# Performance work log

Measured on AMD Instinct MI355X. Metric: run time of the kernel, lower is better.

## Reference

```python
import jax, jax.numpy as jnp
from jax import lax
import numpy as np

PROPRIO = 48
NPTS = 1024
NP_PROX = 512
NP_DIST = 512
HP = 187  # proximal_feature_dim
HD = 64   # distal_feature_dim
B = 2048
NA = 12
ACTOR_DIMS = [PROPRIO + HP + HD, 1024, 512, 256, 128, NA]


def gru_last(x, wih, whh, bih, bhh):
    """torch-style GRU (gate order r,z,n), returns last hidden. x: [B,T,in]."""
    Bx, T, _ = x.shape
    H = whh.shape[1]
    gx = x @ wih.T + bih  # [B,T,3H], input projections precomputed
    def step(h, gxt):
        gh = h @ whh.T + bhh
        r = jax.nn.sigmoid(gxt[:, :H] + gh[:, :H])
        z = jax.nn.sigmoid(gxt[:, H:2 * H] + gh[:, H:2 * H])
        n = jnp.tanh(gxt[:, 2 * H:] + r * gh[:, 2 * H:])
        return (1.0 - z) * n + z * h, None
    h0 = jnp.zeros((Bx, H), x.dtype)
    hT, _ = lax.scan(step, h0, jnp.swapaxes(gx, 0, 1))
    return hT


def _encode(pts, w1, b1, w2, b2):
    h = jax.nn.elu(pts @ w1.T + b1)
    return jax.nn.elu(h @ w2.T + b2)


def _forward(obs, pe_prox_w1, pe_prox_b1, pe_prox_w2, pe_prox_b2,
             pe_dist_w1, pe_dist_b1, pe_dist_w2, pe_dist_b2,
             gru_prox_wih, gru_prox_whh, gru_prox_bih, gru_prox_bhh,
             gru_dist_wih, gru_dist_whh, gru_dist_bih, gru_dist_bhh,
             mem_prox_wih, mem_prox_whh, mem_prox_bih, mem_prox_bhh,
             mem_dist_wih, mem_dist_whh, mem_dist_bih, mem_dist_bhh,
             actor_w0, actor_b0, actor_w1, actor_b1, actor_w2, actor_b2,
             actor_w3, actor_b3, actor_w4, actor_b4,
             prox_idx, dist_idx):
    proprio = obs[:, :PROPRIO]
    lidar = obs[:, PROPRIO:].reshape(obs.shape[0], NPTS, 3)  # history_length=1
    # irregular gather of proximal/distal point subsets (sampling plan buffers)
    prox_enc = _encode(lidar[:, prox_idx], pe_prox_w1, pe_prox_b1, pe_prox_w2, pe_prox_b2)  # [B,512,64]
    dist_enc = _encode(lidar[:, dist_idx], pe_dist_w1, pe_dist_b1, pe_dist_w2, pe_dist_b2)  # [B,512,64]
    # spatial GRUs over the point sequence
    hp = gru_last(prox_enc, gru_prox_wih, gru_prox_whh, gru_prox_bih, gru_prox_bhh)  # [B,187]
    hd = gru_last(dist_enc, gru_dist_wih, gru_dist_whh, gru_dist_bih, gru_dist_bhh)  # [B,64]
    # temporal memory GRUs (single step, zero initial hidden)
    fp = gru_last(hp[:, None, :], mem_prox_wih, mem_prox_whh, mem_prox_bih, mem_prox_bhh)
    fd = gru_last(hd[:, None, :], mem_dist_wih, mem_dist_whh, mem_dist_bih, mem_dist_bhh)
    x = jnp.concatenate([proprio, fp, fd], axis=-1)  # [B,299]
    for w, b in ((actor_w0, actor_b0), (actor_w1, actor_b1), (actor_w2, actor_b2), (actor_w3, actor_b3)):
        x = jax.nn.elu(x @ w.T + b)
    return x @ actor_w4.T + actor_b4  # action mean [B,12]


def setup_inputs() -> dict:
    key = jax.random.key(0)
    ks = iter(jax.random.split(key, 64))
    def n(shape, scale=0.05):
        return (jax.random.normal(next(ks), shape, jnp.float32) * scale)
    inp = {}
    inp["obs"] = jax.random.normal(next(ks), (B, PROPRIO + NPTS * 3), jnp.float32)
    inp["prox_idx"] = jax.random.randint(next(ks), (NP_PROX,), 0, NPTS)
    inp["dist_idx"] = jax.random.randint(next(ks), (NP_DIST,), 0, NPTS)
    for pfx in ("pe_prox", "pe_dist"):
        inp[pfx + "_w1"] = n((64, 3)); inp[pfx + "_b1"] = jnp.zeros((64,), jnp.float32)
        inp[pfx + "_w2"] = n((64, 64)); inp[pfx + "_b2"] = jnp.zeros((64,), jnp.float32)
    for pfx, H, din in (("gru_prox", HP, 64), ("gru_dist", HD, 64), ("mem_prox", HP, HP), ("mem_dist", HD, HD)):
        inp[pfx + "_wih"] = n((3 * H, din)); inp[pfx + "_whh"] = n((3 * H, H))
        inp[pfx + "_bih"] = jnp.zeros((3 * H,), jnp.float32); inp[pfx + "_bhh"] = jnp.zeros((3 * H,), jnp.float32)
    for i, (di, do) in enumerate(zip(ACTOR_DIMS[:-1], ACTOR_DIMS[1:])):
        inp[f"actor_w{i}"] = n((do, di)); inp[f"actor_b{i}"] = jnp.zeros((do,), jnp.float32)
    return inp


def reference(obs, prox_idx, dist_idx,
              pe_prox_w1, pe_prox_b1, pe_prox_w2, pe_prox_b2,
              pe_dist_w1, pe_dist_b1, pe_dist_w2, pe_dist_b2,
              gru_prox_wih, gru_prox_whh, gru_prox_bih, gru_prox_bhh,
              gru_dist_wih, gru_dist_whh, gru_dist_bih, gru_dist_bhh,
              mem_prox_wih, mem_prox_whh, mem_prox_bih, mem_prox_bhh,
              mem_dist_wih, mem_dist_whh, mem_dist_bih, mem_dist_bhh,
              actor_w0, actor_b0, actor_w1, actor_b1, actor_w2, actor_b2,
              actor_w3, actor_b3, actor_w4, actor_b4):
    return _forward(obs, pe_prox_w1, pe_prox_b1, pe_prox_w2, pe_prox_b2,
                    pe_dist_w1, pe_dist_b1, pe_dist_w2, pe_dist_b2,
                    gru_prox_wih, gru_prox_whh, gru_prox_bih, gru_prox_bhh,
                    gru_dist_wih, gru_dist_whh, gru_dist_bih, gru_dist_bhh,
                    mem_prox_wih, mem_prox_whh, mem_prox_bih, mem_prox_bhh,
                    mem_dist_wih, mem_dist_whh, mem_dist_bih, mem_dist_bhh,
                    actor_w0, actor_b0, actor_w1, actor_b1, actor_w2, actor_b2,
                    actor_w3, actor_b3, actor_w4, actor_b4,
                    prox_idx, dist_idx)
```

## Files before the change

kernel.cpp:

```cpp
#include <hip/hip_runtime.h>
#include <stdint.h>

typedef __attribute__((ext_vector_type(8))) short short8;
typedef __attribute__((ext_vector_type(4))) float f32x4;
typedef __attribute__((ext_vector_type(4))) unsigned int u32x4;

#define DEV __device__ __forceinline__

#define L2E 1.4426950408889634f

DEV unsigned short f2bf(float f) {
    union { float f; uint32_t u; } v; v.f = f;
    return (unsigned short)((v.u + 0x7FFFu + ((v.u >> 16) & 1u)) >> 16);
}
DEV uint8_t f2fp8(float f) {
    union { float f; uint32_t u; } v; v.f = f;
    uint32_t s = (v.u >> 24) & 0x80u;
    uint32_t absu = v.u & 0x7FFFFFFFu;
    int E = (int)(absu >> 23);
    if (E >= 135 + 1) return (uint8_t)(s | 0x7E);
    if (E >= 121) {
        uint32_t m = absu & 0x7FFFFFu;
        uint32_t keep = m >> 20;
        uint32_t rest = m & 0xFFFFFu;
        uint32_t rnd = (rest > 0x80000u || (rest == 0x80000u && (keep & 1u))) ? 1u : 0u;
        uint32_t mag = (((uint32_t)(E - 120) << 3) | keep) + rnd;
        if (mag > 0x7Eu) mag = 0x7Eu;
        return (uint8_t)(s | mag);
    }
    float sc = __builtin_fabsf(f) * 512.f;
    uint32_t m8 = (uint32_t)(sc + 0.5f);
    if (m8 > 7u) return (uint8_t)(s | 0x08);
    return (uint8_t)(s | m8);
}
DEV float sig_(float x) {
    return __builtin_amdgcn_rcpf(1.f + __builtin_amdgcn_exp2f(-L2E * x));
}
DEV float tanh_(float x) {
    return 1.f - 2.f * __builtin_amdgcn_rcpf(1.f + __builtin_amdgcn_exp2f(2.f * L2E * x));
}
DEV float elu_(float x) {
    return x > 0.f ? x : __builtin_amdgcn_exp2f(L2E * x) - 1.f;
}
DEV f32x4 splat4(float v) { f32x4 r; r[0]=v; r[1]=v; r[2]=v; r[3]=v; return r; }
DEV void pin(short8& v) { asm volatile("" : "+v"(v)); }
DEV void pinl(long& v)  { asm volatile("" : "+v"(v)); }

struct PJob { const float* s; unsigned short* d; int Hs, NG, Ks, Kd, total; };
struct PJobs { PJob j[12]; };

__global__ __launch_bounds__(256) void pack_all(PJobs P)
{
    PJob jb = P.j[blockIdx.y];
    int e = blockIdx.x * 256 + threadIdx.x;
    if (e >= jb.total) return;
    int n = e / jb.Kd, k = e - n * jb.Kd;
    int g = n / jb.NG, jj = n - g * jb.NG;
    float v = (jj < jb.Hs && k < jb.Ks) ? jb.s[(size_t)(g * jb.Hs + jj) * jb.Ks + k] : 0.f;
    jb.d[e] = f2bf(v);
}

__global__ __launch_bounds__(256) void pack_fp8(const float* __restrict__ src,
                                                uint8_t* __restrict__ dst)
{
    int e = blockIdx.x * 256 + threadIdx.x;
    if (e >= 576 * 64) return;
    int n = e >> 6, k = e & 63;
    int g = n / 192, jj = n - g * 192;
    float v = (jj < 187) ? src[(size_t)(g * 187 + jj) * 64 + k] : 0.f;
    dst[e] = f2fp8(v);
}

__global__ __launch_bounds__(256) void enc_kernel(
    const float* __restrict__ obs, const int* __restrict__ idx,
    const float* __restrict__ w1, const float* __restrict__ b1,
    const unsigned short* __restrict__ w2p, const float* __restrict__ b2,
    uint8_t* __restrict__ enc8)
{
    const int b = blockIdx.x, t0 = blockIdx.y * 64;
    const int tid = threadIdx.x;
    __shared__ __align__(16) float pts[64][4];
    __shared__ float w1s[256];
    __shared__ float b1s[64], b2s[64];
    __shared__ __align__(16) unsigned short h1s[64][72];

    if (tid < 192) w1s[(tid/3)*4 + (tid - (tid/3)*3)] = w1[tid];
    if (tid < 64) { b1s[tid] = b1[tid]; b2s[tid] = b2[tid]; }
    for (int e = tid; e < 192; e += 256) {
        int p = e / 3, c2 = e - p * 3;
        int pi = idx[t0 + p];
        pts[p][c2] = obs[(size_t)b * 3120 + 48 + (size_t)pi * 3 + c2];
    }
    __syncthreads();
#pragma unroll
    for (int r = 0; r < 16; ++r) {
        int e = tid + r * 256;
        int p = e >> 6, ch = e & 63;
        float v = w1s[ch*4]*pts[p][0] + w1s[ch*4+1]*pts[p][1]
                + w1s[ch*4+2]*pts[p][2] + b1s[ch];
        h1s[p][ch] = f2bf(elu_(v));
    }
    __syncthreads();
    const int wave = tid >> 6, lane = tid & 63, quad = lane >> 4, l16 = lane & 15;
#pragma unroll
    for (int ct = 0; ct < 4; ++ct) {
        f32x4 a2 = splat4(0.f);
#pragma unroll
        for (int ks = 0; ks < 2; ++ks) {
            short8 af = *(const short8*)(&h1s[wave*16 + l16][ks*32 + quad*8]);
            short8 bf = *(const short8*)(w2p + (ct*16 + l16)*64 + ks*32 + quad*8);
            a2 = __builtin_amdgcn_mfma_f32_16x16x32_bf16(af, bf, a2, 0, 0, 0);
        }
        int c = ct*16 + l16;
        float b2v = b2s[c];
#pragma unroll
        for (int j = 0; j < 4; ++j) {
            int m = wave*16 + quad*4 + j;
            enc8[((size_t)b*512 + t0 + m)*64 + c] = f2fp8(elu_(a2[j] + b2v));
        }
    }
}

DEV void gru_body_pre(int blk, const uint8_t* __restrict__ enc8,
                      const uint8_t* __restrict__ wih8,
                      const unsigned short* __restrict__ whh,
                      const float* __restrict__ bih, const float* __restrict__ bhh,
                      unsigned short* __restrict__ houtb, char* smem)
{
    constexpr int H = 187, KP = 192, KS = 6, HP8 = 200;
    unsigned short* hlds = (unsigned short*)smem;
    uint8_t* xs = (uint8_t*)(smem + 12800);

    const int tid  = threadIdx.x;
    const int wave = tid >> 6, lane = tid & 63, quad = lane >> 4, l16 = lane & 15;
    const int b0   = blk * 16;
    const int c    = wave * 16 + l16;

    for (int e = tid; e < 2*16*HP8; e += 768) hlds[e] = 0;

    short8 whr[3][KS];
    long   wx8[3][2];
#pragma unroll
    for (int g = 0; g < 3; ++g) {
#pragma unroll
        for (int ks = 0; ks < KS; ++ks)
            whr[g][ks] = *(const short8*)(whh + ((size_t)(g*KP + c))*KP + ks*32 + quad*8);
#pragma unroll
        for (int ks = 0; ks < 2; ++ks)
            wx8[g][ks] = *(const long*)(wih8 + ((size_t)(g*KP + c))*64 + ks*32 + quad*8);
    }
#pragma unroll
    for (int g = 0; g < 3; ++g) {
#pragma unroll
        for (int ks = 0; ks < KS; ++ks) pin(whr[g][ks]);
#pragma unroll
        for (int ks = 0; ks < 2; ++ks)  pinl(wx8[g][ks]);
    }
    float bsr = 0.f, bsz = 0.f, binx = 0.f, bhnn = 0.f;
    if (c < H) {
        bsr  = bih[c]       + bhh[c];
        bsz  = bih[H + c]   + bhh[H + c];
        binx = bih[2*H + c];
        bhnn = bhh[2*H + c];
    }
    float hreg[4] = {0.f, 0.f, 0.f, 0.f};

    u32x4 xq;
    const int xrow = lane >> 2, xseg = lane & 3;
    if (wave == 0) {
        xq = *(const u32x4*)(enc8 + ((size_t)(b0 + xrow)*512 + 0)*64 + xseg*16);
        *(u32x4*)(xs + 0*1280 + xrow*80 + xseg*16) = xq;
        xq = *(const u32x4*)(enc8 + ((size_t)(b0 + xrow)*512 + 1)*64 + xseg*16);
    }
    __syncthreads();

    int cur = 0;
    for (int t = 0; t < 512; ++t) {
        if (wave == 0) {
            *(u32x4*)(xs + ((t+1)&1)*1280 + xrow*80 + xseg*16) = xq;
            int tn = (t + 2 < 512) ? t + 2 : 511;
            xq = *(const u32x4*)(enc8 + ((size_t)(b0 + xrow)*512 + tn)*64 + xseg*16);
        }
        const uint8_t* xsr = xs + (t&1)*1280;
        const unsigned short* hc = hlds + cur * (16*HP8);
        unsigned short*       hn = hlds + (cur ^ 1) * (16*HP8);

        f32x4 acc[4];
        acc[0] = splat4(bsr);
        acc[1] = splat4(bsz);
        acc[2] = splat4(binx);
        acc[3] = splat4(bhnn);
#pragma unroll
        for (int ks = 0; ks < 2; ++ks) {
            long a8 = *(const long*)(xsr + l16*80 + ks*32 + quad*8);
            acc[0] = __builtin_amdgcn_mfma_f32_16x16x32_fp8_fp8(a8, wx8[0][ks], acc[0], 0, 0, 0);
            acc[1] = __builtin_amdgcn_mfma_f32_16x16x32_fp8_fp8(a8, wx8[1][ks], acc[1], 0, 0, 0);
            acc[2] = __builtin_amdgcn_mfma_f32_16x16x32_fp8_fp8(a8, wx8[2][ks], acc[2], 0, 0, 0);
        }
#pragma unroll
        for (int ks = 0; ks < KS; ++ks) {
            short8 ah = *(const short8*)(hc + l16*HP8 + ks*32 + quad*8);
            acc[0] = __builtin_amdgcn_mfma_f32_16x16x32_bf16(ah, whr[0][ks], acc[0], 0, 0, 0);
            acc[1] = __builtin_amdgcn_mfma_f32_16x16x32_bf16(ah, whr[1][ks], acc[1], 0, 0, 0);
            acc[3] = __builtin_amdgcn_mfma_f32_16x16x32_bf16(ah, whr[2][ks], acc[3], 0, 0, 0);
        }
#pragma unroll
        for (int j = 0; j < 4; ++j) {
            int m = quad*4 + j;
            float r  = sig_(acc[0][j]);
            float zg = sig_(acc[1][j]);
            float nn = tanh_(acc[2][j] + r * acc[3][j]);
            float hv = nn + zg * (hreg[j] - nn);
            hreg[j] = hv;
            hn[m*HP8 + c] = f2bf(hv);
        }
        cur ^= 1;
        __syncthreads();
    }
#pragma unroll
    for (int j = 0; j < 4; ++j) {
        int m = quad*4 + j;
        houtb[(size_t)(b0 + m)*KP + c] = (c < H) ? f2bf(hreg[j]) : 0;
    }
}

template<int H, int KP>
DEV void gru_body_fused(int blk,
                  const float* __restrict__ obs, const int* __restrict__ idx,
                  const float* __restrict__ w1, const float* __restrict__ b1,
                  const float* __restrict__ w2, const float* __restrict__ b2,
                  const unsigned short* __restrict__ wih, const unsigned short* __restrict__ whh,
                  const float* __restrict__ bih, const float* __restrict__ bhh,
                  unsigned short* __restrict__ houtb, char* smem)
{
    constexpr int NCT = KP / 16;
    constexpr int KS  = KP / 32;
    constexpr int HP8 = KP + 8;

    unsigned short* hlds = (unsigned short*)(smem);
    unsigned short* xs   = (unsigned short*)(smem + 12800);
    unsigned short* h1s  = (unsigned short*)(smem + 17408);
    unsigned short* w2s  = (unsigned short*)(smem + 22016);
    float* ptsb          = (float*)(smem + 31232);
    float* w1s           = (float*)(smem + 31744);
    float* b1s           = (float*)(smem + 32768);
    float* b2s           = (float*)(smem + 33024);

    const int tid  = threadIdx.x;
    const int wave = tid >> 6, lane = tid & 63, quad = lane >> 4, l16 = lane & 15;
    const int b0   = blk * 16;
    const int ct   = wave;
    const bool act = (ct < NCT);
    const int c    = ct * 16 + l16;

    for (int e = tid; e < 2*16*HP8; e += 768) hlds[e] = 0;
    for (int e = tid; e < 4096; e += 768) { int n = e >> 6, k = e & 63; w2s[n*72 + k] = f2bf(w2[e]); }
    if (tid < 192) w1s[(tid/3)*4 + (tid - (tid/3)*3)] = w1[tid];
    if (tid < 64) { b1s[tid] = b1[tid]; b2s[tid] = b2[tid]; }

    const float* myrow = obs + (size_t)(b0 + (tid & 15)) * 3120 + 48;
    float px = 0.f, py = 0.f, pz = 0.f;
    if (tid < 16) {
        int p0 = idx[0];
        ptsb[tid*4 + 0] = myrow[3*p0 + 0];
        ptsb[tid*4 + 1] = myrow[3*p0 + 1];
        ptsb[tid*4 + 2] = myrow[3*p0 + 2];
        int p1 = idx[1];
        px = myrow[3*p1 + 0]; py = myrow[3*p1 + 1]; pz = myrow[3*p1 + 2];
    }

    short8 whr[3][KS];
    short8 wxr[3][2];
    float bsr = 0.f, bsz = 0.f, binx = 0.f, bhnn = 0.f;
    {
        const int cl = act ? c : l16;
#pragma unroll
        for (int g = 0; g < 3; ++g) {
#pragma unroll
            for (int ks = 0; ks < KS; ++ks)
                whr[g][ks] = *(const short8*)(whh + ((size_t)(g*KP + cl))*KP + ks*32 + quad*8);
#pragma unroll
            for (int ks = 0; ks < 2; ++ks)
                wxr[g][ks] = *(const short8*)(wih + ((size_t)(g*KP + cl))*64 + ks*32 + quad*8);
        }
    }
#pragma unroll
    for (int g = 0; g < 3; ++g) {
#pragma unroll
        for (int ks = 0; ks < KS; ++ks) pin(whr[g][ks]);
#pragma unroll
        for (int ks = 0; ks < 2; ++ks)  pin(wxr[g][ks]);
    }
    if (act && c < H) {
        bsr  = bih[c]       + bhh[c];
        bsz  = bih[H + c]   + bhh[H + c];
        binx = bih[2*H + c];
        bhnn = bhh[2*H + c];
    }
    float hreg[4] = {0.f, 0.f, 0.f, 0.f};

    __syncthreads();

    int cur = 0;
    for (int i = 0; i < 514; ++i) {
        if (i < 512) {
            const float* pt = ptsb + (i & 1) * 64;
            unsigned short* h1w = h1s + (i & 1) * (16*72);
#pragma unroll
            for (int e = tid; e < 1024; e += 768) {
                int p = e >> 6, ch = e & 63;
                float v = w1s[ch*4+0]*pt[p*4+0] + w1s[ch*4+1]*pt[p*4+1]
                        + w1s[ch*4+2]*pt[p*4+2] + b1s[ch];
                h1w[p*72 + ch] = f2bf(elu_(v));
            }
            if (tid < 16) {
                float* dst = ptsb + ((i+1) & 1) * 64 + tid*4;
                dst[0] = px; dst[1] = py; dst[2] = pz;
                int tn = (i + 2 < 512) ? i + 2 : 511;
                int pn = idx[tn];
                px = myrow[3*pn + 0]; py = myrow[3*pn + 1]; pz = myrow[3*pn + 2];
            }
        }
        if (i >= 1 && i < 513 && wave < 4) {
            const unsigned short* h1r = h1s + ((i-1) & 1) * (16*72);
            unsigned short*       xw  = xs  + ((i-1) & 1) * (16*72);
            f32x4 a2 = splat4(0.f);
#pragma unroll
            for (int ks = 0; ks < 2; ++ks) {
                short8 af = *(const short8*)(h1r + l16*72 + ks*32 + quad*8);
                short8 bf = *(const short8*)(w2s + (wave*16 + l16)*72 + ks*32 + quad*8);
                a2 = __builtin_amdgcn_mfma_f32_16x16x32_bf16(af, bf, a2, 0, 0, 0);
            }
            int c2 = wave*16 + l16;
            float b2v = b2s[c2];
#pragma unroll
            for (int j = 0; j < 4; ++j)
                xw[(quad*4 + j)*72 + c2] = f2bf(elu_(a2[j] + b2v));
        }
        if (i >= 2) {
            int t = i - 2;
            const unsigned short* xsr = xs + (t & 1) * (16*72);
            const unsigned short* hc  = hlds + cur * (16*HP8);
            unsigned short*       hn  = hlds + (cur ^ 1) * (16*HP8);
            if (act) {
                f32x4 acc[4];
                acc[0] = splat4(bsr);
                acc[1] = splat4(bsz);
                acc[2] = splat4(binx);
                acc[3] = splat4(bhnn);
#pragma unroll
                for (int ks = 0; ks < 2; ++ks) {
                    short8 xf = *(const short8*)(xsr + l16*72 + ks*32 + quad*8);
                    acc[0] = __builtin_amdgcn_mfma_f32_16x16x32_bf16(xf, wxr[0][ks], acc[0], 0, 0, 0);
                    acc[1] = __builtin_amdgcn_mfma_f32_16x16x32_bf16(xf, wxr[1][ks], acc[1], 0, 0, 0);
                    acc[2] = __builtin_amdgcn_mfma_f32_16x16x32_bf16(xf, wxr[2][ks], acc[2], 0, 0, 0);
                }
#pragma unroll
                for (int ks = 0; ks < KS; ++ks) {
                    short8 ah = *(const short8*)(hc + l16*HP8 + ks*32 + quad*8);
                    acc[0] = __builtin_amdgcn_mfma_f32_16x16x32_bf16(ah, whr[0][ks], acc[0], 0, 0, 0);
                    acc[1] = __builtin_amdgcn_mfma_f32_16x16x32_bf16(ah, whr[1][ks], acc[1], 0, 0, 0);
                    acc[3] = __builtin_amdgcn_mfma_f32_16x16x32_bf16(ah, whr[2][ks], acc[3], 0, 0, 0);
                }
#pragma unroll
                for (int j = 0; j < 4; ++j) {
                    int m = quad*4 + j;
                    float r  = sig_(acc[0][j]);
                    float zg = sig_(acc[1][j]);
                    float nn = tanh_(acc[2][j] + r * acc[3][j]);
                    float hv = nn + zg * (hreg[j] - nn);
                    hreg[j] = hv;
                    hn[m*HP8 + c] = f2bf(hv);
                }
            }
            cur ^= 1;
        }
        __syncthreads();
    }

    if (act)
#pragma unroll
        for (int j = 0; j < 4; ++j) {
            int m = quad*4 + j;
            houtb[(size_t)(b0 + m)*KP + c] = (c < H) ? f2bf(hreg[j]) : 0;
        }
}

__global__ __launch_bounds__(768) void gru_kernel(
    int mode,
    const float* __restrict__ obs,
    const int* __restrict__ prox_idx, const int* __restrict__ dist_idx,
    const uint8_t* __restrict__ encp8, const uint8_t* __restrict__ wihp8,
    const float* __restrict__ w1p, const float* __restrict__ b1p,
    const float* __restrict__ w2p, const float* __restrict__ b2p,
    const float* __restrict__ w1d, const float* __restrict__ b1d,
    const float* __restrict__ w2d, const float* __restrict__ b2d,
    const unsigned short* __restrict__ wihp, const unsigned short* __restrict__ whhp,
    const unsigned short* __restrict__ wihd, const unsigned short* __restrict__ whhd,
    const float* __restrict__ bihp, const float* __restrict__ bhhp,
    const float* __restrict__ bihd, const float* __restrict__ bhhd,
    unsigned short* __restrict__ hpb, unsigned short* __restrict__ hdb)
{
    __shared__ __align__(16) char smem[33280];
    if (blockIdx.x < 128) {
        if (mode == 0)
            gru_body_pre(blockIdx.x, encp8, wihp8, whhp, bihp, bhhp, hpb, smem);
        else
            gru_body_fused<187, 192>(blockIdx.x, obs, prox_idx, w1p, b1p, w2p, b2p,
                                     wihp, whhp, bihp, bhhp, hpb, smem);
    } else {
        gru_body_fused<64, 64>(blockIdx.x - 128, obs, dist_idx, w1d, b1d, w2d, b2d,
                               wihd, whhd, bihd, bhhd, hdb, smem);
    }
}

__global__ __launch_bounds__(256) void bgemm_kernel(
    const unsigned short* __restrict__ A, const unsigned short* __restrict__ B,
    const float* __restrict__ bias, void* __restrict__ C,
    int Kp, int Np, int Nstore, int mode)
{
    __shared__ __align__(16) unsigned short Asl[64*40];
    __shared__ __align__(16) unsigned short Bsl[64*40];
    const int tid = threadIdx.x;
    const int wave = tid >> 6, lane = tid & 63, quad = lane >> 4, l16 = lane & 15;
    const int n0 = blockIdx.x * 64, m0 = blockIdx.y * 64;
    const int r = tid >> 2, sg = (tid & 3) * 8;

    f32x4 acc[4];
#pragma unroll
    for (int nt = 0; nt < 4; ++nt) acc[nt] = splat4(0.f);

    for (int k0 = 0; k0 < Kp; k0 += 32) {
        short8 av = *(const short8*)(A + (size_t)(m0 + r)*Kp + k0 + sg);
        short8 bv;
        if (n0 + r < Np) bv = *(const short8*)(B + (size_t)(n0 + r)*Kp + k0 + sg);
        else { short8 z; for (int q = 0; q < 8; ++q) z[q] = 0; bv = z; }
        *(short8*)(Asl + r*40 + sg) = av;
        *(short8*)(Bsl + r*40 + sg) = bv;
        __syncthreads();
        short8 af = *(const short8*)(Asl + (wave*16 + l16)*40 + quad*8);
#pragma unroll
        for (int nt = 0; nt < 4; ++nt) {
            short8 bf = *(const short8*)(Bsl + (nt*16 + l16)*40 + quad*8);
            acc[nt] = __builtin_amdgcn_mfma_f32_16x16x32_bf16(af, bf, acc[nt], 0, 0, 0);
        }
        __syncthreads();
    }
#pragma unroll
    for (int nt = 0; nt < 4; ++nt) {
        int n = n0 + nt*16 + l16;
        float bv = (bias && n < Np) ? bias[n] : 0.f;
#pragma unroll
        for (int j = 0; j < 4; ++j) {
            int m = m0 + wave*16 + quad*4 + j;
            float v = acc[nt][j] + bv;
            if (mode == 1) {
                ((unsigned short*)C)[(size_t)m*Np + n] = f2bf(elu_(v));
            } else {
                if (n < Nstore) ((float*)C)[(size_t)m*Nstore + n] = v;
            }
        }
    }
}

__global__ __launch_bounds__(256) void memcat_kernel(
    const float* __restrict__ obs, const float* __restrict__ Gp, const float* __restrict__ Gd,
    const float* __restrict__ mbip, const float* __restrict__ mbhp,
    const float* __restrict__ mbid, const float* __restrict__ mbhd,
    unsigned short* __restrict__ x0b)
{
    int i = blockIdx.x * 256 + threadIdx.x;
    if (i >= 2048 * 320) return;
    int b = i / 320, cc = i - b * 320;
    float v;
    if (cc < 48) {
        v = obs[(size_t)b*3120 + cc];
    } else if (cc < 235) {
        int j = cc - 48;
        float dr = Gp[(size_t)b*576 + j];
        float dz = Gp[(size_t)b*576 + 192 + j];
        float dn = Gp[(size_t)b*576 + 384 + j];
        float r  = sig_(dr + mbip[j] + mbhp[j]);
        float zg = sig_(dz + mbip[187+j] + mbhp[187+j]);
        float nn = tanh_(dn + mbip[374+j] + r * mbhp[374+j]);
        v = (1.f - zg) * nn;
    } else if (cc < 299) {
        int j = cc - 235;
        float dr = Gd[(size_t)b*192 + j];
        float dz = Gd[(size_t)b*192 + 64 + j];
        float dn = Gd[(size_t)b*192 + 128 + j];
        float r  = sig_(dr + mbid[j] + mbhd[j]);
        float zg = sig_(dz + mbid[64+j] + mbhd[64+j]);
        float nn = tanh_(dn + mbid[128+j] + r * mbhd[128+j]);
        v = (1.f - zg) * nn;
    } else {
        v = 0.f;
    }
    x0b[i] = f2bf(v);
}

extern "C" void kernel_launch(void* const* d_in, const int* in_sizes, int n_in,
                              void* d_out, int out_size, void* d_ws, size_t ws_size,
                              hipStream_t stream)
{
    (void)in_sizes; (void)n_in; (void)out_size;
    const float* obs        = (const float*)d_in[0];
    const int*   prox_idx   = (const int*)d_in[1];
    const int*   dist_idx   = (const int*)d_in[2];
    const float* pe_prox_w1 = (const float*)d_in[3];
    const float* pe_prox_b1 = (const float*)d_in[4];
    const float* pe_prox_w2 = (const float*)d_in[5];
    const float* pe_prox_b2 = (const float*)d_in[6];
    const float* pe_dist_w1 = (const float*)d_in[7];
    const float* pe_dist_b1 = (const float*)d_in[8];
    const float* pe_dist_w2 = (const float*)d_in[9];
    const float* pe_dist_b2 = (const float*)d_in[10];
    const float* gp_wih = (const float*)d_in[11];
    const float* gp_whh = (const float*)d_in[12];
    const float* gp_bih = (const float*)d_in[13];
    const float* gp_bhh = (const float*)d_in[14];
    const float* gd_wih = (const float*)d_in[15];
    const float* gd_whh = (const float*)d_in[16];
    const float* gd_bih = (const float*)d_in[17];
    const float* gd_bhh = (const float*)d_in[18];
    const float* mp_wih = (const float*)d_in[19];
    const float* mp_bih = (const float*)d_in[21];
    const float* mp_bhh = (const float*)d_in[22];
    const float* md_wih = (const float*)d_in[23];
    const float* md_bih = (const float*)d_in[25];
    const float* md_bhh = (const float*)d_in[26];
    const float* aw0 = (const float*)d_in[27]; const float* ab0 = (const float*)d_in[28];
    const float* aw1 = (const float*)d_in[29]; const float* ab1 = (const float*)d_in[30];
    const float* aw2 = (const float*)d_in[31]; const float* ab2 = (const float*)d_in[32];
    const float* aw3 = (const float*)d_in[33]; const float* ab3 = (const float*)d_in[34];
    const float* aw4 = (const float*)d_in[35]; const float* ab4 = (const float*)d_in[36];
    float* out = (float*)d_out;

    char* ws = (char*)d_ws;
    size_t off = 0;
    auto alloc = [&](size_t bytes) -> char* {
        char* p = ws + off;
        off = (off + bytes + 255) & ~(size_t)255;
        return p;
    };
    unsigned short* wih_p = (unsigned short*)alloc(36864*2);
    unsigned short* whh_p = (unsigned short*)alloc(110592*2);
    unsigned short* wih_d = (unsigned short*)alloc(12288*2);
    unsigned short* whh_d = (unsigned short*)alloc(12288*2);
    unsigned short* mw_p  = (unsigned short*)alloc(110592*2);
    unsigned short* mw_d  = (unsigned short*)alloc(12288*2);
    unsigned short* w0p   = (unsigned short*)alloc((size_t)1024*320*2);
    unsigned short* w1p   = (unsigned short*)alloc((size_t)512*1024*2);
    unsigned short* w2p   = (unsigned short*)alloc((size_t)256*512*2);
    unsigned short* w3p   = (unsigned short*)alloc((size_t)128*256*2);
    unsigned short* w4p   = (unsigned short*)alloc((size_t)16*128*2);
    unsigned short* w2e   = (unsigned short*)alloc(4096*2);
    uint8_t* wih8         = (uint8_t*)alloc(576*64);
    unsigned short* hpb   = (unsigned short*)alloc((size_t)2048*192*2);
    unsigned short* hdb   = (unsigned short*)alloc((size_t)2048*64*2);
    float* Gp             = (float*)alloc((size_t)2048*576*4);
    float* Gd             = (float*)alloc((size_t)2048*192*4);
    unsigned short* x0b   = (unsigned short*)alloc((size_t)2048*320*2);
    unsigned short* a1b   = (unsigned short*)alloc((size_t)2048*1024*2);
    unsigned short* a2b   = (unsigned short*)alloc((size_t)2048*512*2);
    unsigned short* a3b   = (unsigned short*)alloc((size_t)2048*256*2);
    unsigned short* a4b   = (unsigned short*)alloc((size_t)2048*128*2);
    uint8_t* enc8         = (uint8_t*)alloc((size_t)2048*512*64);
    const int mode = (off <= ws_size) ? 0 : 1;

    PJobs P;
    P.j[0]  = { gp_wih, wih_p, 187, 192, 64, 64, 36864 };
    P.j[1]  = { gp_whh, whh_p, 187, 192, 187, 192, 110592 };
    P.j[2]  = { gd_wih, wih_d, 64, 64, 64, 64, 12288 };
    P.j[3]  = { gd_whh, whh_d, 64, 64, 64, 64, 12288 };
    P.j[4]  = { mp_wih, mw_p, 187, 192, 187, 192, 110592 };
    P.j[5]  = { md_wih, mw_d, 64, 64, 64, 64, 12288 };
    P.j[6]  = { aw0, w0p, 1024, 1024, 299, 320, 327680 };
    P.j[7]  = { aw1, w1p, 512, 512, 1024, 1024, 524288 };
    P.j[8]  = { aw2, w2p, 256, 256, 512, 512, 131072 };
    P.j[9]  = { aw3, w3p, 128, 128, 256, 256, 32768 };
    P.j[10] = { aw4, w4p, 12, 16, 128, 128, 2048 };
    P.j[11] = { pe_prox_w2, w2e, 64, 64, 64, 64, 4096 };
    pack_all<<<dim3(2048, 12), 256, 0, stream>>>(P);

    if (mode == 0) {
        pack_fp8<<<144, 256, 0, stream>>>(gp_wih, wih8);
        enc_kernel<<<dim3(2048, 8), 256, 0, stream>>>(
            obs, prox_idx, pe_prox_w1, pe_prox_b1, w2e, pe_prox_b2, enc8);
    }

    gru_kernel<<<256, 768, 0, stream>>>(
        mode, obs, prox_idx, dist_idx, enc8, wih8,
        pe_prox_w1, pe_prox_b1, pe_prox_w2, pe_prox_b2,
        pe_dist_w1, pe_dist_b1, pe_dist_w2, pe_dist_b2,
        wih_p, whh_p, wih_d, whh_d,
        gp_bih, gp_bhh, gd_bih, gd_bhh, hpb, hdb);

    bgemm_kernel<<<dim3(9, 32), 256, 0, stream>>>(hpb, mw_p, nullptr, Gp, 192, 576, 576, 0);
    bgemm_kernel<<<dim3(3, 32), 256, 0, stream>>>(hdb, mw_d, nullptr, Gd, 64, 192, 192, 0);
    memcat_kernel<<<2560, 256, 0, stream>>>(obs, Gp, Gd, mp_bih, mp_bhh, md_bih, md_bhh, x0b);

    bgemm_kernel<<<dim3(16, 32), 256, 0, stream>>>(x0b, w0p, ab0, a1b, 320, 1024, 1024, 1);
    bgemm_kernel<<<dim3(8,  32), 256, 0, stream>>>(a1b, w1p, ab1, a2b, 1024, 512, 512, 1);
    bgemm_kernel<<<dim3(4,  32), 256, 0, stream>>>(a2b, w2p, ab2, a3b, 512, 256, 256, 1);
    bgemm_kernel<<<dim3(2,  32), 256, 0, stream>>>(a3b, w3p, ab3, a4b, 256, 128, 128, 1);
    bgemm_kernel<<<dim3(1,  32), 256, 0, stream>>>(a4b, w4p, ab4, out, 128, 16, 12, 0);
}
```

Measured before the change: 851.0 us.

## Fold activation scales into GRU weights and fuse memory GRU with concat

Pre-multiplies the GRU gate weights and biases by -log2(e) or 2·log2(e) while packing, so each recurrent step's sigmoid and tanh reduce to exp2 plus reciprocal with no extra multiply. Hidden states are converted to bf16 two at a time with a packed convert when the compiler offers it. The two memory-GRU GEMMs and the concat kernel are merged into one memfuse kernel that applies the gates straight from the MFMA accumulators, which removes the fp32 Gp and Gd round trip and two launches. The fp8 weight pack moves into pack_all. Rounding changes slightly because the scales are applied before bf16 and fp8 quantization.

```diff
diff --git a/kernel.cpp b/kernel.cpp
--- a/kernel.cpp
+++ b/kernel.cpp
@@ -12,13 +12,28 @@
 DEV unsigned short f2bf(float f) {
     union { float f; uint32_t u; } v; v.f = f;
     return (unsigned short)((v.u + 0x7FFFu + ((v.u >> 16) & 1u)) >> 16);
+}
+#if defined(__has_builtin)
+#if __has_builtin(__builtin_amdgcn_cvt_pk_bf16_f32)
+#define HAS_PK_BF16 1
+#endif
+#endif
+DEV uint32_t pk_bf16(float a, float b) {
+#ifdef HAS_PK_BF16
+    typedef __attribute__((ext_vector_type(2))) __bf16 bf2;
+    union { bf2 v; uint32_t u; } cv;
+    cv.v = __builtin_amdgcn_cvt_pk_bf16_f32(a, b);
+    return cv.u;
+#else
+    return (uint32_t)f2bf(a) | ((uint32_t)f2bf(b) << 16);
+#endif
 }
 DEV uint8_t f2fp8(float f) {
     union { float f; uint32_t u; } v; v.f = f;
     uint32_t s = (v.u >> 24) & 0x80u;
     uint32_t absu = v.u & 0x7FFFFFFFu;
     int E = (int)(absu >> 23);
-    if (E >= 135 + 1) return (uint8_t)(s | 0x7E);
+    if (E >= 136) return (uint8_t)(s | 0x7E);
     if (E >= 121) {
         uint32_t m = absu & 0x7FFFFFu;
         uint32_t keep = m >> 20;
@@ -33,12 +48,10 @@
     if (m8 > 7u) return (uint8_t)(s | 0x08);
     return (uint8_t)(s | m8);
 }
-DEV float sig_(float x) {
-    return __builtin_amdgcn_rcpf(1.f + __builtin_amdgcn_exp2f(-L2E * x));
-}
-DEV float tanh_(float x) {
-    return 1.f - 2.f * __builtin_amdgcn_rcpf(1.f + __builtin_amdgcn_exp2f(2.f * L2E * x));
-}
+DEV float rcp1pe_(float x) {
+    return __builtin_amdgcn_rcpf(1.f + __builtin_amdgcn_exp2f(x));
+}
+DEV float sig_(float x) { return rcp1pe_(-L2E * x); }
 DEV float elu_(float x) {
     return x > 0.f ? x : __builtin_amdgcn_exp2f(L2E * x) - 1.f;
 }
@@ -46,8 +59,8 @@
 DEV void pin(short8& v) { asm volatile("" : "+v"(v)); }
 DEV void pinl(long& v)  { asm volatile("" : "+v"(v)); }
 
-struct PJob { const float* s; unsigned short* d; int Hs, NG, Ks, Kd, total; };
-struct PJobs { PJob j[12]; };
+struct PJob { const float* s; void* d; int Hs, NG, Ks, Kd, total; float s0, s1, s2; int fmt; };
+struct PJobs { PJob j[13]; };
 
 __global__ __launch_bounds__(256) void pack_all(PJobs P)
 {
@@ -56,19 +69,10 @@
     if (e >= jb.total) return;
     int n = e / jb.Kd, k = e - n * jb.Kd;
     int g = n / jb.NG, jj = n - g * jb.NG;
-    float v = (jj < jb.Hs && k < jb.Ks) ? jb.s[(size_t)(g * jb.Hs + jj) * jb.Ks + k] : 0.f;
-    jb.d[e] = f2bf(v);
-}
-
-__global__ __launch_bounds__(256) void pack_fp8(const float* __restrict__ src,
-                                                uint8_t* __restrict__ dst)
-{
-    int e = blockIdx.x * 256 + threadIdx.x;
-    if (e >= 576 * 64) return;
-    int n = e >> 6, k = e & 63;
-    int g = n / 192, jj = n - g * 192;
-    float v = (jj < 187) ? src[(size_t)(g * 187 + jj) * 64 + k] : 0.f;
-    dst[e] = f2fp8(v);
+    float sc = (g == 0) ? jb.s0 : ((g == 1) ? jb.s1 : jb.s2);
+    float v = (jj < jb.Hs && k < jb.Ks) ? jb.s[(size_t)(g * jb.Hs + jj) * jb.Ks + k] * sc : 0.f;
+    if (jb.fmt) ((uint8_t*)jb.d)[e] = f2fp8(v);
+    else        ((unsigned short*)jb.d)[e] = f2bf(v);
 }
 
 __global__ __launch_bounds__(256) void enc_kernel(
@@ -158,10 +162,10 @@
     }
     float bsr = 0.f, bsz = 0.f, binx = 0.f, bhnn = 0.f;
     if (c < H) {
-        bsr  = bih[c]       + bhh[c];
-        bsz  = bih[H + c]   + bhh[H + c];
-        binx = bih[2*H + c];
-        bhnn = bhh[2*H + c];
+        bsr  = -L2E * (bih[c]       + bhh[c]);
+        bsz  = -L2E * (bih[H + c]   + bhh[H + c]);
+        binx = 2.f * L2E * bih[2*H + c];
+        bhnn = 2.f * L2E * bhh[2*H + c];
     }
     float hreg[4] = {0.f, 0.f, 0.f, 0.f};
 
@@ -204,16 +208,21 @@
             acc[1] = __builtin_amdgcn_mfma_f32_16x16x32_bf16(ah, whr[1][ks], acc[1], 0, 0, 0);
             acc[3] = __builtin_amdgcn_mfma_f32_16x16x32_bf16(ah, whr[2][ks], acc[3], 0, 0, 0);
         }
+        float hv[4];
 #pragma unroll
         for (int j = 0; j < 4; ++j) {
-            int m = quad*4 + j;
-            float r  = sig_(acc[0][j]);
-            float zg = sig_(acc[1][j]);
-            float nn = tanh_(acc[2][j] + r * acc[3][j]);
-            float hv = nn + zg * (hreg[j] - nn);
-            hreg[j] = hv;
-            hn[m*HP8 + c] = f2bf(hv);
-        }
+            float r  = rcp1pe_(acc[0][j]);
+            float zg = rcp1pe_(acc[1][j]);
+            float nn = __builtin_fmaf(-2.f, rcp1pe_(__builtin_fmaf(r, acc[3][j], acc[2][j])), 1.f);
+            hv[j] = __builtin_fmaf(zg, hreg[j] - nn, nn);
+            hreg[j] = hv[j];
+        }
+        uint32_t p01 = pk_bf16(hv[0], hv[1]);
+        uint32_t p23 = pk_bf16(hv[2], hv[3]);
+        hn[(quad*4+0)*HP8 + c] = (unsigned short)p01;
+        hn[(quad*4+1)*HP8 + c] = (unsigned short)(p01 >> 16);
+        hn[(quad*4+2)*HP8 + c] = (unsigned short)p23;
+        hn[(quad*4+3)*HP8 + c] = (unsigned short)(p23 >> 16);
         cur ^= 1;
         __syncthreads();
     }
@@ -292,10 +301,10 @@
         for (int ks = 0; ks < 2; ++ks)  pin(wxr[g][ks]);
     }
     if (act && c < H) {
-        bsr  = bih[c]       + bhh[c];
-        bsz  = bih[H + c]   + bhh[H + c];
-        binx = bih[2*H + c];
-        bhnn = bhh[2*H + c];
+        bsr  = -L2E * (bih[c]       + bhh[c]);
+        bsz  = -L2E * (bih[H + c]   + bhh[H + c]);
+        binx = 2.f * L2E * bih[2*H + c];
+        bhnn = 2.f * L2E * bhh[2*H + c];
     }
     float hreg[4] = {0.f, 0.f, 0.f, 0.f};
 
@@ -362,16 +371,21 @@
                     acc[1] = __builtin_amdgcn_mfma_f32_16x16x32_bf16(ah, whr[1][ks], acc[1], 0, 0, 0);
                     acc[3] = __builtin_amdgcn_mfma_f32_16x16x32_bf16(ah, whr[2][ks], acc[3], 0, 0, 0);
                 }
+                float hv[4];
 #pragma unroll
                 for (int j = 0; j < 4; ++j) {
-                    int m = quad*4 + j;
-                    float r  = sig_(acc[0][j]);
-                    float zg = sig_(acc[1][j]);
-                    float nn = tanh_(acc[2][j] + r * acc[3][j]);
-                    float hv = nn + zg * (hreg[j] - nn);
-                    hreg[j] = hv;
-                    hn[m*HP8 + c] = f2bf(hv);
+                    float r  = rcp1pe_(acc[0][j]);
+                    float zg = rcp1pe_(acc[1][j]);
+                    float nn = __builtin_fmaf(-2.f, rcp1pe_(__builtin_fmaf(r, acc[3][j], acc[2][j])), 1.f);
+                    hv[j] = __builtin_fmaf(zg, hreg[j] - nn, nn);
+                    hreg[j] = hv[j];
                 }
+                uint32_t p01 = pk_bf16(hv[0], hv[1]);
+                uint32_t p23 = pk_bf16(hv[2], hv[3]);
+                hn[(quad*4+0)*HP8 + c] = (unsigned short)p01;
+                hn[(quad*4+1)*HP8 + c] = (unsigned short)(p01 >> 16);
+                hn[(quad*4+2)*HP8 + c] = (unsigned short)p23;
+                hn[(quad*4+3)*HP8 + c] = (unsigned short)(p23 >> 16);
             }
             cur ^= 1;
         }
@@ -414,6 +428,89 @@
     }
 }
 
+__global__ __launch_bounds__(256) void memfuse_kernel(
+    const float* __restrict__ obs,
+    const unsigned short* __restrict__ hpb, const unsigned short* __restrict__ hdb,
+    const unsigned short* __restrict__ mwp, const unsigned short* __restrict__ mwd,
+    const float* __restrict__ mbip, const float* __restrict__ mbhp,
+    const float* __restrict__ mbid, const float* __restrict__ mbhd,
+    unsigned short* __restrict__ x0b)
+{
+    __shared__ __align__(16) unsigned short Asl[64*40];
+    __shared__ __align__(16) unsigned short Bsl[3][64*40];
+    const int tid = threadIdx.x;
+    const int wave = tid >> 6, lane = tid & 63, quad = lane >> 4, l16 = lane & 15;
+    const int z = blockIdx.x, m0 = blockIdx.y * 64;
+    const bool isp = (z < 3);
+    const unsigned short* A = isp ? hpb : hdb;
+    const unsigned short* B = isp ? mwp : mwd;
+    const float* bi = isp ? mbip : mbid;
+    const float* bh = isp ? mbhp : mbhd;
+    const int Kp = isp ? 192 : 64;
+    const int Hh = isp ? 187 : 64;
+    const int jb = isp ? z * 64 : 0;
+    const int cbase = isp ? 48 : 235;
+    const int r = tid >> 2, sg = (tid & 3) * 8;
+
+    f32x4 acc[3][4];
+#pragma unroll
+    for (int g = 0; g < 3; ++g)
+#pragma unroll
+        for (int nt = 0; nt < 4; ++nt) acc[g][nt] = splat4(0.f);
+
+    for (int k0 = 0; k0 < Kp; k0 += 32) {
+        *(short8*)(Asl + r*40 + sg) = *(const short8*)(A + (size_t)(m0 + r)*Kp + k0 + sg);
+#pragma unroll
+        for (int g = 0; g < 3; ++g)
+            *(short8*)(Bsl[g] + r*40 + sg) =
+                *(const short8*)(B + (size_t)(g*Kp + jb + r)*Kp + k0 + sg);
+        __syncthreads();
+        short8 af = *(const short8*)(Asl + (wave*16 + l16)*40 + quad*8);
+#pragma unroll
+        for (int g = 0; g < 3; ++g)
+#pragma unroll
+            for (int nt = 0; nt < 4; ++nt) {
+                short8 bf = *(const short8*)(Bsl[g] + (nt*16 + l16)*40 + quad*8);
+                acc[g][nt] = __builtin_amdgcn_mfma_f32_16x16x32_bf16(af, bf, acc[g][nt], 0, 0, 0);
+            }
+        __syncthreads();
+    }
+#pragma unroll
+    for (int nt = 0; nt < 4; ++nt) {
+        int j = jb + nt*16 + l16;
+        bool valid = (j < Hh);
+        float br = 0.f, bz = 0.f, bnx = 0.f, bnh = 0.f;
+        if (valid) {
+            br  = -L2E * (bi[j] + bh[j]);
+            bz  = -L2E * (bi[Hh + j] + bh[Hh + j]);
+            bnx = 2.f * L2E * bi[2*Hh + j];
+            bnh = 2.f * L2E * bh[2*Hh + j];
+        }
+#pragma unroll
+        for (int jj = 0; jj < 4; ++jj) {
+            int m = m0 + wave*16 + quad*4 + jj;
+            float rr = rcp1pe_(acc[0][nt][jj] + br);
+            float zz = rcp1pe_(acc[1][nt][jj] + bz);
+            float tt = __builtin_fmaf(rr, bnh, acc[2][nt][jj] + bnx);
+            float nn = __builtin_fmaf(-2.f, rcp1pe_(tt), 1.f);
+            float v  = (1.f - zz) * nn;
+            if (valid) x0b[(size_t)m*320 + cbase + j] = f2bf(v);
+        }
+    }
+    if (z == 0) {
+        for (int e = tid; e < 64*48; e += 256) {
+            int m = m0 + e / 48, cc = e - (e / 48) * 48;
+            x0b[(size_t)m*320 + cc] = f2bf(obs[(size_t)m*3120 + cc]);
+        }
+    }
+    if (z == 3) {
+        for (int e = tid; e < 64*21; e += 256) {
+            int m = m0 + e / 21, cc = 299 + (e - (e / 21) * 21);
+            x0b[(size_t)m*320 + cc] = 0;
+        }
+    }
+}
+
 __global__ __launch_bounds__(256) void bgemm_kernel(
     const unsigned short* __restrict__ A, const unsigned short* __restrict__ B,
     const float* __restrict__ bias, void* __restrict__ C,
@@ -434,7 +531,7 @@
         short8 av = *(const short8*)(A + (size_t)(m0 + r)*Kp + k0 + sg);
         short8 bv;
         if (n0 + r < Np) bv = *(const short8*)(B + (size_t)(n0 + r)*Kp + k0 + sg);
-        else { short8 z; for (int q = 0; q < 8; ++q) z[q] = 0; bv = z; }
+        else { short8 zz; for (int q = 0; q < 8; ++q) zz[q] = 0; bv = zz; }
         *(short8*)(Asl + r*40 + sg) = av;
         *(short8*)(Bsl + r*40 + sg) = bv;
         __syncthreads();
@@ -461,42 +558,6 @@
             }
         }
     }
-}
-
-__global__ __launch_bounds__(256) void memcat_kernel(
-    const float* __restrict__ obs, const float* __restrict__ Gp, const float* __restrict__ Gd,
-    const float* __restrict__ mbip, const float* __restrict__ mbhp,
-    const float* __restrict__ mbid, const float* __restrict__ mbhd,
-    unsigned short* __restrict__ x0b)
-{
-    int i = blockIdx.x * 256 + threadIdx.x;
-    if (i >= 2048 * 320) return;
-    int b = i / 320, cc = i - b * 320;
-    float v;
-    if (cc < 48) {
-        v = obs[(size_t)b*3120 + cc];
-    } else if (cc < 235) {
-        int j = cc - 48;
-        float dr = Gp[(size_t)b*576 + j];
-        float dz = Gp[(size_t)b*576 + 192 + j];
-        float dn = Gp[(size_t)b*576 + 384 + j];
-        float r  = sig_(dr + mbip[j] + mbhp[j]);
-        float zg = sig_(dz + mbip[187+j] + mbhp[187+j]);
-        float nn = tanh_(dn + mbip[374+j] + r * mbhp[374+j]);
-        v = (1.f - zg) * nn;
-    } else if (cc < 299) {
-        int j = cc - 235;
-        float dr = Gd[(size_t)b*192 + j];
-        float dz = Gd[(size_t)b*192 + 64 + j];
-        float dn = Gd[(size_t)b*192 + 128 + j];
-        float r  = sig_(dr + mbid[j] + mbhd[j]);
-        float zg = sig_(dz + mbid[64+j] + mbhd[64+j]);
-        float nn = tanh_(dn + mbid[128+j] + r * mbhd[128+j]);
-        v = (1.f - zg) * nn;
-    } else {
-        v = 0.f;
-    }
-    x0b[i] = f2bf(v);
 }
 
 extern "C" void kernel_launch(void* const* d_in, const int* in_sizes, int n_in,
@@ -558,8 +619,6 @@
     uint8_t* wih8         = (uint8_t*)alloc(576*64);
     unsigned short* hpb   = (unsigned short*)alloc((size_t)2048*192*2);
     unsigned short* hdb   = (unsigned short*)alloc((size_t)2048*64*2);
-    float* Gp             = (float*)alloc((size_t)2048*576*4);
-    float* Gd             = (float*)alloc((size_t)2048*192*4);
     unsigned short* x0b   = (unsigned short*)alloc((size_t)2048*320*2);
     unsigned short* a1b   = (unsigned short*)alloc((size_t)2048*1024*2);
     unsigned short* a2b   = (unsigned short*)alloc((size_t)2048*512*2);
@@ -568,23 +627,24 @@
     uint8_t* enc8         = (uint8_t*)alloc((size_t)2048*512*64);
     const int mode = (off <= ws_size) ? 0 : 1;
 
+    const float SR = -L2E, SN = 2.f * L2E;
     PJobs P;
-    P.j[0]  = { gp_wih, wih_p, 187, 192, 64, 64, 36864 };
-    P.j[1]  = { gp_whh, whh_p, 187, 192, 187, 192, 110592 };
-    P.j[2]  = { gd_wih, wih_d, 64, 64, 64, 64, 12288 };
-    P.j[3]  = { gd_whh, whh_d, 64, 64, 64, 64, 12288 };
-    P.j[4]  = { mp_wih, mw_p, 187, 192, 187, 192, 110592 };
-    P.j[5]  = { md_wih, mw_d, 64, 64, 64, 64, 12288 };
-    P.j[6]  = { aw0, w0p, 1024, 1024, 299, 320, 327680 };
-    P.j[7]  = { aw1, w1p, 512, 512, 1024, 1024, 524288 };
-    P.j[8]  = { aw2, w2p, 256, 256, 512, 512, 131072 };
-    P.j[9]  = { aw3, w3p, 128, 128, 256, 256, 32768 };
-    P.j[10] = { aw4, w4p, 12, 16, 128, 128, 2048 };
-    P.j[11] = { pe_prox_w2, w2e, 64, 64, 64, 64, 4096 };
-    pack_all<<<dim3(2048, 12), 256, 0, stream>>>(P);
+    P.j[0]  = { gp_wih, wih_p, 187, 192, 64, 64, 36864, SR, SR, SN, 0 };
+    P.j[1]  = { gp_whh, whh_p, 187, 192, 187, 192, 110592, SR, SR, SN, 0 };
+    P.j[2]  = { gd_wih, wih_d, 64, 64, 64, 64, 12288, SR, SR, SN, 0 };
+    P.j[3]  = { gd_whh, whh_d, 64, 64, 64, 64, 12288, SR, SR, SN, 0 };
+    P.j[4]  = { mp_wih, mw_p, 187, 192, 187, 192, 110592, SR, SR, SN, 0 };
+    P.j[5]  = { md_wih, mw_d, 64, 64, 64, 64, 12288, SR, SR, SN, 0 };
+    P.j[6]  = { aw0, w0p, 1024, 1024, 299, 320, 327680, 1.f, 1.f, 1.f, 0 };
+    P.j[7]  = { aw1, w1p, 512, 512, 1024, 1024, 524288, 1.f, 1.f, 1.f, 0 };
+    P.j[8]  = { aw2, w2p, 256, 256, 512, 512, 131072, 1.f, 1.f, 1.f, 0 };
+    P.j[9]  = { aw3, w3p, 128, 128, 256, 256, 32768, 1.f, 1.f, 1.f, 0 };
+    P.j[10] = { aw4, w4p, 12, 16, 128, 128, 2048, 1.f, 1.f, 1.f, 0 };
+    P.j[11] = { pe_prox_w2, w2e, 64, 64, 64, 64, 4096, 1.f, 1.f, 1.f, 0 };
+    P.j[12] = { gp_wih, wih8, 187, 192, 64, 64, 36864, SR, SR, SN, 1 };
+    pack_all<<<dim3(2048, 13), 256, 0, stream>>>(P);
 
     if (mode == 0) {
-        pack_fp8<<<144, 256, 0, stream>>>(gp_wih, wih8);
         enc_kernel<<<dim3(2048, 8), 256, 0, stream>>>(
             obs, prox_idx, pe_prox_w1, pe_prox_b1, w2e, pe_prox_b2, enc8);
     }
@@ -596,9 +656,8 @@
         wih_p, whh_p, wih_d, whh_d,
         gp_bih, gp_bhh, gd_bih, gd_bhh, hpb, hdb);
 
-    bgemm_kernel<<<dim3(9, 32), 256, 0, stream>>>(hpb, mw_p, nullptr, Gp, 192, 576, 576, 0);
-    bgemm_kernel<<<dim3(3, 32), 256, 0, stream>>>(hdb, mw_d, nullptr, Gd, 64, 192, 192, 0);
-    memcat_kernel<<<2560, 256, 0, stream>>>(obs, Gp, Gd, mp_bih, mp_bhh, md_bih, md_bhh, x0b);
+    memfuse_kernel<<<dim3(4, 32), 256, 0, stream>>>(
+        obs, hpb, hdb, mw_p, mw_d, mp_bih, mp_bhh, md_bih, md_bhh, x0b);
 
     bgemm_kernel<<<dim3(16, 32), 256, 0, stream>>>(x0b, w0p, ab0, a1b, 320, 1024, 1024, 1);
     bgemm_kernel<<<dim3(8,  32), 256, 0, stream>>>(a1b, w1p, ab1, a2b, 1024, 512, 512, 1);
```

Result: faster. 811.0 us (-4.7%).
